# Performance work log

Measured on AMD Instinct MI355X. Metric: run time of the kernel, lower is better.

The kernel has to match this reference:

```python
import jax, jax.numpy as jnp
import numpy as np

OUT, IN, G, TOK = 4096, 4096, 16, 8192


def setup_inputs() -> dict:
    key = jax.random.key(0)
    k1, k2, k3, k4 = jax.random.split(key, 4)
    x = jax.random.normal(k1, (TOK, IN), dtype=jnp.float32)
    # packed int4 pairs: each byte holds two 4-bit values (low nibble, high nibble)
    weight_q4 = jax.random.randint(k2, (OUT * IN // G, G // 2), 0, 256, dtype=jnp.int32)
    # per-group abs-max normalization, strictly positive
    weight_norm = jax.random.uniform(k3, (OUT * IN // G, 1), dtype=jnp.float16, minval=0.01, maxval=1.0)
    bias = jax.random.normal(k4, (OUT,), dtype=jnp.float32) * 0.01
    return {"x": x, "weight_q4": weight_q4, "weight_norm": weight_norm, "bias": bias}


def _dequant_4bit(weight_q4, weight_norm):
    # unpack nibbles: even positions = low nibble, odd positions = high nibble
    low = weight_q4 & 15
    high = (weight_q4 >> 4) & 15
    q8 = jnp.stack([low, high], axis=-1).reshape(weight_q4.shape[0], -1)  # [n_groups, G]
    norm = weight_norm.astype(jnp.float32)                                 # [n_groups, 1]
    w = (q8.astype(jnp.float32) / 15.0) * 2.0 * norm - norm               # [-norm, +norm]
    return w.reshape(OUT, IN)


def reference(x, weight_q4, weight_norm, bias):
    W = _dequant_4bit(weight_q4, weight_norm)  # [OUT, IN] fp32
    return x @ W.T + bias                      # [TOK, OUT]
```

## Files before the change

### kernel.cpp

```cpp
#include <hip/hip_runtime.h>
#include <hip/hip_fp16.h>

#define M_TOK 8192
#define N_OUT 4096
#define K_IN  4096
#define GRP   16

typedef __bf16 bf16x8 __attribute__((ext_vector_type(8)));
typedef float  f32x4  __attribute__((ext_vector_type(4)));
typedef unsigned short ushort8 __attribute__((ext_vector_type(8)));

__device__ __forceinline__ float bfbits(unsigned short h) {
    unsigned int u = ((unsigned int)h) << 16;
    return __builtin_bit_cast(float, u);
}

#define GLDS16(gp, sp) __builtin_amdgcn_global_load_lds(                      \
        (const __attribute__((address_space(1))) void*)(gp),                  \
        (__attribute__((address_space(3))) void*)(sp), 16, 0, 0)

__device__ __forceinline__ void detect_block(const void* __restrict__ xv,
                                             const void* __restrict__ nrmv,
                                             const void* __restrict__ biasv,
                                             int* s_modes) {
    const int tid = threadIdx.x;
    if (tid < 64) {
        const unsigned short* px = (const unsigned short*)xv;
        unsigned short hx = px[tid * 2];
        int ex = (hx >> 7) & 0xFF;
        bool xok = ((ex >= 64 && ex <= 134) || (hx & 0x7FFF) == 0);
        unsigned long long xb = __ballot(xok);

        const unsigned short* pn = (const unsigned short*)nrmv;
        unsigned short hn = pn[tid & 31];
        float v16 = __half2float(__builtin_bit_cast(__half, hn));
        float vbf = bfbits(hn);
        unsigned long long b16 = __ballot(v16 > 0.0085f && v16 < 1.02f);
        unsigned long long bbf = __ballot(vbf > 0.0085f && vbf < 1.02f);

        const unsigned short* pb = (const unsigned short*)biasv;
        unsigned short hb = pb[tid * 2];
        int eb = (hb >> 7) & 0xFF;
        bool bok = ((eb >= 64 && eb <= 134) || (hb & 0x7FFF) == 0);
        unsigned long long bb = __ballot(bok);

        if (tid == 0) {
            s_modes[0] = (xb == ~0ULL) ? 1 : 0;
            s_modes[1] = (b16 == ~0ULL) ? 0 : ((bbf == ~0ULL) ? 1 : 2);
            s_modes[2] = (bb == ~0ULL) ? 1 : 0;
        }
    }
    __syncthreads();
}

__global__ __launch_bounds__(256) void prep_all(const void* __restrict__ xv,
                                                const int* __restrict__ q4,
                                                const void* __restrict__ nrmv,
                                                const void* __restrict__ biasv,
                                                __bf16* __restrict__ W,
                                                __bf16* __restrict__ X) {
    __shared__ int s_modes[3];
    detect_block(xv, nrmv, biasv, s_modes);
    const int tid = threadIdx.x;

    if (blockIdx.x < 4096) {
        const int nmode = s_modes[1];
        const int t = blockIdx.x * 256 + tid;
        const int4* qp = (const int4*)q4 + (size_t)t * 2;
        int4 a4 = qp[0], c4 = qp[1];
        float nm;
        if (nmode == 0)      nm = __half2float(((const __half*)nrmv)[t]);
        else if (nmode == 1) nm = bfbits(((const unsigned short*)nrmv)[t]);
        else                 nm = ((const float*)nrmv)[t];
        float s = nm * (2.0f / 15.0f);
        int qs[8] = {a4.x, a4.y, a4.z, a4.w, c4.x, c4.y, c4.z, c4.w};
        bf16x8 v0, v1;
#pragma unroll
        for (int u = 0; u < 8; ++u) {
            float lo = fmaf((float)(qs[u] & 15), s, -nm);
            float hi = fmaf((float)((qs[u] >> 4) & 15), s, -nm);
            if (u < 4) { v0[2 * u] = (__bf16)lo; v0[2 * u + 1] = (__bf16)hi; }
            else       { v1[2 * (u - 4)] = (__bf16)lo; v1[2 * (u - 4) + 1] = (__bf16)hi; }
        }
        bf16x8* wp = (bf16x8*)(W + (size_t)t * 16);
        wp[0] = v0; wp[1] = v1;
    } else {
        if (s_modes[0] == 1) return;
        const int bx = blockIdx.x - 4096;
        const int total8 = M_TOK * K_IN / 8;
        const int stride = 2048 * 256;
        for (int i = bx * 256 + tid; i < total8; i += stride) {
            const float4* fp = (const float4*)xv + (size_t)i * 2;
            float4 f0 = fp[0], f1 = fp[1];
            bf16x8 u;
            u[0] = (__bf16)f0.x; u[1] = (__bf16)f0.y; u[2] = (__bf16)f0.z; u[3] = (__bf16)f0.w;
            u[4] = (__bf16)f1.x; u[5] = (__bf16)f1.y; u[6] = (__bf16)f1.z; u[7] = (__bf16)f1.w;
            *(bf16x8*)(X + (size_t)i * 8) = u;
        }
    }
}

#define PHASE(d, h, p, WT, ...) do {                                          \
    const __bf16* Ar_ = As + (d)*16384 + aregion;                             \
    const __bf16* Br_ = Bs + (d)*16384 + bregion;                             \
    bf16x8 af_[4][2], bv_[2][2];                                              \
    _Pragma("unroll")                                                         \
    for (int ii = 0; ii < 4; ++ii) {                                          \
        const int R_ = (((h)*4 + ii)*16 + r) * 64;                            \
        af_[ii][0] = *(const bf16x8*)(Ar_ + R_ + qs8);                        \
        af_[ii][1] = *(const bf16x8*)(Ar_ + R_ + 32 + qs8);                   \
    }                                                                         \
    _Pragma("unroll")                                                         \
    for (int jj = 0; jj < 2; ++jj) {                                          \
        const int RB_ = (brow0 + ((p)*2 + jj)*16 + r) * 64;                   \
        bv_[jj][0] = *(const bf16x8*)(Br_ + RB_ + qs8);                       \
        bv_[jj][1] = *(const bf16x8*)(Br_ + RB_ + 32 + qs8);                  \
    }                                                                         \
    __VA_ARGS__                                                               \
    if ((WT) == 2) asm volatile("s_waitcnt vmcnt(2)" ::: "memory");           \
    if ((WT) == 1) asm volatile("s_waitcnt vmcnt(0)" ::: "memory");           \
    __builtin_amdgcn_s_barrier();                                             \
    asm volatile("s_waitcnt lgkmcnt(0)" ::: "memory");                        \
    __builtin_amdgcn_sched_barrier(0);                                        \
    __builtin_amdgcn_s_setprio(1);                                            \
    _Pragma("unroll")                                                         \
    for (int ii = 0; ii < 4; ++ii)                                            \
    _Pragma("unroll")                                                         \
    for (int jj = 0; jj < 2; ++jj) {                                          \
        acc[(h)*4+ii][(p)*2+jj] = __builtin_amdgcn_mfma_f32_16x16x32_bf16(    \
            af_[ii][0], bv_[jj][0], acc[(h)*4+ii][(p)*2+jj], 0, 0, 0);        \
        acc[(h)*4+ii][(p)*2+jj] = __builtin_amdgcn_mfma_f32_16x16x32_bf16(    \
            af_[ii][1], bv_[jj][1], acc[(h)*4+ii][(p)*2+jj], 0, 0, 0);        \
    }                                                                         \
    __builtin_amdgcn_s_setprio(0);                                            \
    __builtin_amdgcn_s_barrier();                                             \
} while (0)

__global__ __launch_bounds__(512, 1) void gemm8ph(
        const void* __restrict__ xv, const __bf16* __restrict__ Xws,
        const __bf16* __restrict__ W, const void* __restrict__ nrmv,
        const void* __restrict__ biasv, float* __restrict__ out) {
    __shared__ __align__(16) __bf16 As[2 * 16384];
    __shared__ __align__(16) __bf16 Bs[2 * 16384];
    __shared__ int s_modes[3];

    detect_block(xv, nrmv, biasv, s_modes);
    const int xmode = s_modes[0];
    const int bmode = s_modes[2];
    const __bf16* A = xmode ? (const __bf16*)xv : Xws;

    const int bid = blockIdx.x;
    const int n0 = (bid & 15) * 256;
    const int m0 = (bid >> 4) * 256;

    const int tid = threadIdx.x;
    const int w  = tid >> 6;
    const int l  = tid & 63;
    const int r  = l & 15;
    const int q  = l >> 4;
    const int wm = (w >> 2) * 128;
    const int wn = (w & 3) * 64;
    const int qs8 = (q ^ (((r >> 2) & 1) << 1)) * 8;
    const int aregion = (w >> 2) * 8192;
    const int bregion = ((w & 3) >> 1) * 8192;
    const int brow0   = (w & 1) * 64;

    const int srow = tid >> 3;
    const int scol = ((tid & 7) ^ (((tid >> 5) & 1) << 1)) * 8;
    const __bf16* gA = A + (size_t)(m0 + srow) * K_IN + scol;
    const __bf16* gB = W + (size_t)(n0 + srow) * K_IN + scol;

    auto stgA = [&](int d, int hi, int kt) {
        const size_t ko = (size_t)kt * 64;
        GLDS16(gA + (size_t)(hi * 64) * K_IN + ko,       As + d * 16384 + hi * 4096 + tid * 8);
        GLDS16(gA + (size_t)(hi * 64 + 128) * K_IN + ko, As + d * 16384 + 8192 + hi * 4096 + tid * 8);
    };
    auto stgB = [&](int d, int hi, int kt) {
        const size_t ko = (size_t)kt * 64;
        GLDS16(gB + (size_t)(hi * 128) * K_IN + ko,      Bs + d * 16384 + hi * 8192 + tid * 8);
        GLDS16(gB + (size_t)(hi * 128 + 64) * K_IN + ko, Bs + d * 16384 + hi * 8192 + 4096 + tid * 8);
    };

    f32x4 acc[8][4];
#pragma unroll
    for (int j = 0; j < 4; ++j) {
        const int bidx = n0 + wn + j * 16 + r;
        float bv = (bmode == 0) ? ((const float*)biasv)[bidx]
                                : bfbits(((const unsigned short*)biasv)[bidx]);
#pragma unroll
        for (int i = 0; i < 8; ++i) {
            acc[i][j][0] = bv; acc[i][j][1] = bv; acc[i][j][2] = bv; acc[i][j][3] = bv;
        }
    }

    stgA(0, 0, 0); stgA(0, 1, 0); stgB(0, 0, 0); stgB(0, 1, 0);
    stgA(1, 0, 1);
    asm volatile("s_waitcnt vmcnt(2)" ::: "memory");
    __builtin_amdgcn_s_barrier();

    for (int i = 0; i < 32; ++i) {
        const int k1 = 2 * i + 1, k2 = 2 * i + 2, k3 = 2 * i + 3;
        const bool st = (i < 31);
        const int wt4 = st ? 2 : 1;
        const int wt8 = st ? 2 : 0;

        PHASE(0, 0, 0, 0, stgA(1, 1, k1); );
        PHASE(0, 0, 1, 0, stgB(1, 0, k1); );
        PHASE(0, 1, 0, 0, stgB(1, 1, k1); );
        PHASE(0, 1, 1, wt4, if (st) stgA(0, 0, k2); );
        PHASE(1, 0, 0, 0, if (st) stgA(0, 1, k2); );
        PHASE(1, 0, 1, 0, if (st) stgB(0, 0, k2); );
        PHASE(1, 1, 0, 0, if (st) stgB(0, 1, k2); );
        PHASE(1, 1, 1, wt8, if (st) stgA(1, 0, k3); );
    }

#pragma unroll
    for (int i = 0; i < 8; ++i) {
        const int row = m0 + wm + i * 16 + q * 4;
#pragma unroll
        for (int j = 0; j < 4; ++j) {
            const int col = n0 + wn + j * 16 + r;
            float* p = out + (size_t)row * N_OUT + col;
            p[0 * N_OUT] = acc[i][j][0];
            p[1 * N_OUT] = acc[i][j][1];
            p[2 * N_OUT] = acc[i][j][2];
            p[3 * N_OUT] = acc[i][j][3];
        }
    }
}

__global__ __launch_bounds__(256, 2) void gemm_fused(
        const void* __restrict__ xv,
        const int* __restrict__ q4, const void* __restrict__ nrmv,
        const void* __restrict__ biasv, float* __restrict__ out) {
    __shared__ __align__(16) __bf16 As[128 * 32];
    __shared__ __align__(16) __bf16 Bs[128 * 32];
    __shared__ int s_modes[3];

    detect_block(xv, nrmv, biasv, s_modes);
    const int tid = threadIdx.x;
    const int xmode = s_modes[0];
    const int nmode = s_modes[1];
    const int bmode = s_modes[2];

    const int bid = blockIdx.x;
    const int n0 = (bid & 31) * 128;
    const int m0 = (bid >> 5) * 128;

    const int w  = tid >> 6;
    const int l  = tid & 63;
    const int r  = l & 15;
    const int q  = l >> 4;
    const int wm = (w >> 1) * 64;
    const int wn = (w & 1) * 64;

    const int arow = tid >> 1;
    const int acol = (tid & 1) * 16;
    const size_t aoff = (size_t)(m0 + arow) * K_IN + acol;

    const int brow = tid >> 1;
    const int bgc  = tid & 1;

    f32x4 acc[4][4];
#pragma unroll
    for (int j = 0; j < 4; ++j) {
        const int bidx = n0 + wn + j * 16 + r;
        float bv = (bmode == 0) ? ((const float*)biasv)[bidx]
                                : bfbits(((const unsigned short*)biasv)[bidx]);
#pragma unroll
        for (int i = 0; i < 4; ++i) {
            acc[i][j][0] = bv; acc[i][j][1] = bv; acc[i][j][2] = bv; acc[i][j][3] = bv;
        }
    }

    for (int k0 = 0; k0 < K_IN; k0 += 32) {
        __syncthreads();
        {
            const int g = (n0 + brow) * (K_IN / GRP) + (k0 >> 4) + bgc;
            const int4* qp = (const int4*)q4 + (size_t)g * 2;
            int4 a4 = qp[0], c4 = qp[1];
            float nm;
            if (nmode == 0)      nm = __half2float(((const __half*)nrmv)[g]);
            else if (nmode == 1) nm = bfbits(((const unsigned short*)nrmv)[g]);
            else                 nm = ((const float*)nrmv)[g];
            float s = nm * (2.0f / 15.0f);
            int qs[8] = {a4.x, a4.y, a4.z, a4.w, c4.x, c4.y, c4.z, c4.w};
            bf16x8 v0, v1;
#pragma unroll
            for (int u = 0; u < 8; ++u) {
                float lo = fmaf((float)(qs[u] & 15), s, -nm);
                float hi = fmaf((float)((qs[u] >> 4) & 15), s, -nm);
                if (u < 4) { v0[2 * u] = (__bf16)lo; v0[2 * u + 1] = (__bf16)hi; }
                else       { v1[2 * (u - 4)] = (__bf16)lo; v1[2 * (u - 4) + 1] = (__bf16)hi; }
            }
            bf16x8* bp = (bf16x8*)(Bs + brow * 32 + bgc * 16);
            bp[0] = v0; bp[1] = v1;
        }

        if (xmode == 0) {
            const float4* ap = (const float4*)((const float*)xv + aoff + k0);
            float4 f0 = ap[0], f1 = ap[1], f2 = ap[2], f3 = ap[3];
            bf16x8 u0, u1;
            u0[0] = (__bf16)f0.x; u0[1] = (__bf16)f0.y; u0[2] = (__bf16)f0.z; u0[3] = (__bf16)f0.w;
            u0[4] = (__bf16)f1.x; u0[5] = (__bf16)f1.y; u0[6] = (__bf16)f1.z; u0[7] = (__bf16)f1.w;
            u1[0] = (__bf16)f2.x; u1[1] = (__bf16)f2.y; u1[2] = (__bf16)f2.z; u1[3] = (__bf16)f2.w;
            u1[4] = (__bf16)f3.x; u1[5] = (__bf16)f3.y; u1[6] = (__bf16)f3.z; u1[7] = (__bf16)f3.w;
            bf16x8* asp = (bf16x8*)(As + arow * 32 + acol);
            asp[0] = u0; asp[1] = u1;
        } else {
            const ushort8* ap = (const ushort8*)((const unsigned short*)xv + aoff + k0);
            ushort8 u0 = ap[0], u1 = ap[1];
            bf16x8* asp = (bf16x8*)(As + arow * 32 + acol);
            asp[0] = __builtin_bit_cast(bf16x8, u0);
            asp[1] = __builtin_bit_cast(bf16x8, u1);
        }

        __syncthreads();

        bf16x8 af[4], bf[4];
#pragma unroll
        for (int i = 0; i < 4; ++i)
            af[i] = *(const bf16x8*)(As + (wm + i * 16 + r) * 32 + q * 8);
#pragma unroll
        for (int j = 0; j < 4; ++j)
            bf[j] = *(const bf16x8*)(Bs + (wn + j * 16 + r) * 32 + q * 8);

#pragma unroll
        for (int i = 0; i < 4; ++i)
#pragma unroll
            for (int j = 0; j < 4; ++j)
                acc[i][j] = __builtin_amdgcn_mfma_f32_16x16x32_bf16(
                    af[i], bf[j], acc[i][j], 0, 0, 0);
    }

#pragma unroll
    for (int i = 0; i < 4; ++i) {
        const int row = m0 + wm + i * 16 + q * 4;
#pragma unroll
        for (int j = 0; j < 4; ++j) {
            const int col = n0 + wn + j * 16 + r;
            float* p = out + (size_t)row * N_OUT + col;
            p[0 * N_OUT] = acc[i][j][0];
            p[1 * N_OUT] = acc[i][j][1];
            p[2 * N_OUT] = acc[i][j][2];
            p[3 * N_OUT] = acc[i][j][3];
        }
    }
}

extern "C" void kernel_launch(void* const* d_in, const int* in_sizes, int n_in,
                              void* d_out, int out_size, void* d_ws, size_t ws_size,
                              hipStream_t stream) {
    const void* x    = d_in[0];
    const int*  q4   = (const int*)d_in[1];
    const void* nrm  = d_in[2];
    const void* bias = d_in[3];
    float*      out  = (float*)d_out;

    const size_t X_OFF = (size_t)N_OUT * K_IN * 2;
    const size_t NEED  = X_OFF + (size_t)M_TOK * K_IN * 2;

    if (ws_size >= NEED) {
        __bf16* W = (__bf16*)d_ws;
        __bf16* X = (__bf16*)((char*)d_ws + X_OFF);

        prep_all<<<4096 + 2048, 256, 0, stream>>>(x, q4, nrm, bias, W, X);
        gemm8ph<<<(M_TOK / 256) * (N_OUT / 256), 512, 0, stream>>>(
            x, X, W, nrm, bias, out);
    } else {
        gemm_fused<<<(M_TOK / 128) * (N_OUT / 128), 256, 0, stream>>>(
            x, q4, nrm, bias, out);
    }
}
```

Before: 578.8 us.

## Reuse register fragments across phases, widen LDS swizzle, and deepen global prefetch

The 8-phase GEMM loop now keeps A fragments and two B fragment buffers in registers across phases, so each phase issues fewer LDS reads. The LDS XOR swizzle is widened from a 2-bit pattern to a full 3-bit row-based pattern to cut bank conflicts. Global-to-LDS staging is reordered so more loads are in flight, with waits at vmcnt(6) instead of vmcnt(2). This raises register pressure and makes correctness depend on the new staging order matching the buffer reuse.

```diff
diff --git a/kernel.cpp b/kernel.cpp
--- a/kernel.cpp
+++ b/kernel.cpp
@@ -100,25 +100,27 @@
     }
 }
 
-#define PHASE(d, h, p, WT, ...) do {                                          \
-    const __bf16* Ar_ = As + (d)*16384 + aregion;                             \
-    const __bf16* Br_ = Bs + (d)*16384 + bregion;                             \
-    bf16x8 af_[4][2], bv_[2][2];                                              \
+#define READ_A(d, h) do {                                                     \
     _Pragma("unroll")                                                         \
     for (int ii = 0; ii < 4; ++ii) {                                          \
-        const int R_ = (((h)*4 + ii)*16 + r) * 64;                            \
-        af_[ii][0] = *(const bf16x8*)(Ar_ + R_ + qs8);                        \
-        af_[ii][1] = *(const bf16x8*)(Ar_ + R_ + 32 + qs8);                   \
-    }                                                                         \
+        const __bf16* b_ = As + (d)*16384 + aregion                           \
+                         + ((((h)*4 + ii)*16 + r) * 64);                      \
+        af[ii][0] = *(const bf16x8*)(b_ + qs8a);                              \
+        af[ii][1] = *(const bf16x8*)(b_ + (qs8a ^ 32));                       \
+    } } while (0)
+
+#define READ_B(d, p, BV) do {                                                 \
     _Pragma("unroll")                                                         \
     for (int jj = 0; jj < 2; ++jj) {                                          \
-        const int RB_ = (brow0 + ((p)*2 + jj)*16 + r) * 64;                   \
-        bv_[jj][0] = *(const bf16x8*)(Br_ + RB_ + qs8);                       \
-        bv_[jj][1] = *(const bf16x8*)(Br_ + RB_ + 32 + qs8);                  \
-    }                                                                         \
-    __VA_ARGS__                                                               \
-    if ((WT) == 2) asm volatile("s_waitcnt vmcnt(2)" ::: "memory");           \
-    if ((WT) == 1) asm volatile("s_waitcnt vmcnt(0)" ::: "memory");           \
+        const __bf16* b_ = Bs + (d)*16384 + bregion                           \
+                         + ((brow0 + ((p)*2 + jj)*16 + r) * 64);              \
+        BV[jj][0] = *(const bf16x8*)(b_ + qs8a);                              \
+        BV[jj][1] = *(const bf16x8*)(b_ + (qs8a ^ 32));                       \
+    } } while (0)
+
+#define SYNC_MFMA(WT, h, p, BV) do {                                          \
+    if ((WT) == 6) asm volatile("s_waitcnt vmcnt(6)" ::: "memory");           \
+    if ((WT) == 0) asm volatile("s_waitcnt vmcnt(0)" ::: "memory");           \
     __builtin_amdgcn_s_barrier();                                             \
     asm volatile("s_waitcnt lgkmcnt(0)" ::: "memory");                        \
     __builtin_amdgcn_sched_barrier(0);                                        \
@@ -128,9 +130,9 @@
     _Pragma("unroll")                                                         \
     for (int jj = 0; jj < 2; ++jj) {                                          \
         acc[(h)*4+ii][(p)*2+jj] = __builtin_amdgcn_mfma_f32_16x16x32_bf16(    \
-            af_[ii][0], bv_[jj][0], acc[(h)*4+ii][(p)*2+jj], 0, 0, 0);        \
+            af[ii][0], BV[jj][0], acc[(h)*4+ii][(p)*2+jj], 0, 0, 0);          \
         acc[(h)*4+ii][(p)*2+jj] = __builtin_amdgcn_mfma_f32_16x16x32_bf16(    \
-            af_[ii][1], bv_[jj][1], acc[(h)*4+ii][(p)*2+jj], 0, 0, 0);        \
+            af[ii][1], BV[jj][1], acc[(h)*4+ii][(p)*2+jj], 0, 0, 0);          \
     }                                                                         \
     __builtin_amdgcn_s_setprio(0);                                            \
     __builtin_amdgcn_s_barrier();                                             \
@@ -160,13 +162,13 @@
     const int q  = l >> 4;
     const int wm = (w >> 2) * 128;
     const int wn = (w & 3) * 64;
-    const int qs8 = (q ^ (((r >> 2) & 1) << 1)) * 8;
+    const int qs8a = (q ^ (r & 7)) * 8;
     const int aregion = (w >> 2) * 8192;
     const int bregion = ((w & 3) >> 1) * 8192;
     const int brow0   = (w & 1) * 64;
 
     const int srow = tid >> 3;
-    const int scol = ((tid & 7) ^ (((tid >> 5) & 1) << 1)) * 8;
+    const int scol = ((tid & 7) ^ ((tid >> 3) & 7)) * 8;
     const __bf16* gA = A + (size_t)(m0 + srow) * K_IN + scol;
     const __bf16* gB = W + (size_t)(n0 + srow) * K_IN + scol;
 
@@ -193,25 +195,47 @@
         }
     }
 
-    stgA(0, 0, 0); stgA(0, 1, 0); stgB(0, 0, 0); stgB(0, 1, 0);
-    stgA(1, 0, 1);
-    asm volatile("s_waitcnt vmcnt(2)" ::: "memory");
+    bf16x8 af[4][2], bva[2][2], bvb[2][2];
+
+    stgA(0, 0, 0); stgB(0, 0, 0); stgB(0, 1, 0); stgA(0, 1, 0);
+    stgA(1, 0, 1); stgB(1, 0, 1); stgB(1, 1, 1);
+    asm volatile("s_waitcnt vmcnt(6)" ::: "memory");
     __builtin_amdgcn_s_barrier();
 
     for (int i = 0; i < 32; ++i) {
         const int k1 = 2 * i + 1, k2 = 2 * i + 2, k3 = 2 * i + 3;
         const bool st = (i < 31);
-        const int wt4 = st ? 2 : 1;
-        const int wt8 = st ? 2 : 0;
-
-        PHASE(0, 0, 0, 0, stgA(1, 1, k1); );
-        PHASE(0, 0, 1, 0, stgB(1, 0, k1); );
-        PHASE(0, 1, 0, 0, stgB(1, 1, k1); );
-        PHASE(0, 1, 1, wt4, if (st) stgA(0, 0, k2); );
-        PHASE(1, 0, 0, 0, if (st) stgA(0, 1, k2); );
-        PHASE(1, 0, 1, 0, if (st) stgB(0, 0, k2); );
-        PHASE(1, 1, 0, 0, if (st) stgB(0, 1, k2); );
-        PHASE(1, 1, 1, wt8, if (st) stgA(1, 0, k3); );
+        const int wt = st ? 6 : 0;
+
+        READ_A(0, 0); READ_B(0, 0, bva);
+        stgA(1, 1, k1);
+        SYNC_MFMA(-1, 0, 0, bva);
+
+        READ_B(0, 1, bvb);
+        if (st) stgA(0, 0, k2);
+        SYNC_MFMA(-1, 0, 1, bvb);
+
+        READ_A(0, 1);
+        if (st) stgB(0, 0, k2);
+        SYNC_MFMA(-1, 1, 0, bva);
+
+        if (st) stgB(0, 1, k2);
+        SYNC_MFMA(wt, 1, 1, bvb);
+
+        READ_A(1, 0); READ_B(1, 0, bva);
+        if (st) stgA(0, 1, k2);
+        SYNC_MFMA(-1, 0, 0, bva);
+
+        READ_B(1, 1, bvb);
+        if (st) stgA(1, 0, k3);
+        SYNC_MFMA(-1, 0, 1, bvb);
+
+        READ_A(1, 1);
+        if (st) stgB(1, 0, k3);
+        SYNC_MFMA(-1, 1, 0, bva);
+
+        if (st) stgB(1, 1, k3);
+        SYNC_MFMA(wt, 1, 1, bvb);
     }
 
 #pragma unroll
```

Measured after the change: 520.3 us. -10.1%, faster.
